# Kernel optimization log

Hardware: AMD Instinct MI355X
Metric: run time of the kernel (lower is better)

Reference implementation:

```python
import jax, jax.numpy as jnp
import numpy as np

B, T, N, A, D, S, E, H = 32, 64, 16, 20, 128, 32, 64, 256  # batch, time, n_agents, n_actions, state_dim, sample_size, embed_dim, hypernet_embed


def _lin(k, fi, fo):
    return jax.random.normal(k, (fi, fo), jnp.float32) / np.sqrt(fi)


def setup_inputs() -> dict:
    key = jax.random.key(0)
    ks = jax.random.split(key, 16)
    batch = B * T
    states = jax.random.normal(ks[0], (B, T, D), jnp.float32)
    a_idx = jax.random.randint(ks[1], (B, T, N), 0, A)
    actions = jax.nn.one_hot(a_idx, A, dtype=jnp.float32)
    agent_qs = jax.random.normal(ks[2], (B, T, N), jnp.float32)
    max_filter = jnp.zeros((B, T, N), jnp.float32)
    # random agent permutations (torch.multinomial without replacement)
    grand_coalitions = jnp.argsort(jax.random.uniform(ks[3], (batch * S, N)), axis=1).astype(jnp.int32)
    return {
        "states": states, "actions": actions, "agent_qs": agent_qs,
        "max_filter": max_filter, "grand_coalitions": grand_coalitions,
        # hyper_w_1: Linear(D,H) -> ReLU -> Linear(H, E*2A)
        "W1a": _lin(ks[4], D, H), "b1a": jnp.zeros((H,), jnp.float32),
        "W1b": _lin(ks[5], H, E * 2 * A), "b1b": jnp.zeros((E * 2 * A,), jnp.float32),
        # hyper_b_1: Linear(D,E)
        "Wb": _lin(ks[6], D, E), "bb": jnp.zeros((E,), jnp.float32),
        # hyper_w_final: Linear(D,H) -> ReLU -> Linear(H,E)
        "Wfa": _lin(ks[7], D, H), "bfa": jnp.zeros((H,), jnp.float32),
        "Wfb": _lin(ks[8], H, E), "bfb": jnp.zeros((E,), jnp.float32),
        # V: Linear(D,E) -> ReLU -> Linear(E,1)
        "Wv1": _lin(ks[9], D, E), "bv1": jnp.zeros((E,), jnp.float32),
        "Wv2": _lin(ks[10], E, 1), "bv2": jnp.zeros((1,), jnp.float32),
    }


def reference(states, actions, agent_qs, max_filter, grand_coalitions,
              W1a, b1a, W1b, b1b, Wb, bb, Wfa, bfa, Wfb, bfb, Wv1, bv1, Wv2, bv2):
    b, t = states.shape[0], states.shape[1]
    batch = b * t
    n, a = actions.shape[2], actions.shape[3]
    s = grand_coalitions.shape[0] // batch
    e = Wb.shape[1]

    st = states.reshape(batch, -1)                      # [batch, D]
    act = actions.reshape(batch, n, a)                  # [batch, N, A]
    gc = grand_coalitions.reshape(batch, s, n)          # [batch, S, N]

    # individual_map one-hot + tril matmul => subcoalition; mask = sub - ind = (j < gc)
    j = jnp.arange(n)
    sub = (j[None, None, None, :] <= gc[..., None]).astype(st.dtype)   # [batch,S,N,N]
    ind = (j[None, None, None, :] == gc[..., None]).astype(st.dtype)
    mask = sub - ind                                                    # [batch,S,i,j]

    # gathered (permuted) actions: perm_act[b,s,j,:] = act[b, gc[b,s,j], :]
    perm_act = act[jnp.arange(batch)[:, None, None], gc]                # [batch,S,N,A]

    # mean over coalition axis j of masked actions, times coalition size, mean over samples
    numer = jnp.einsum('bsij,bsja->bsia', mask, perm_act)               # sum_j masked actions
    cnt = mask.sum(-1)                                                  # [batch,S,N]
    coal = ((numer / n) * cnt[..., None]).mean(axis=1)                  # [batch,N,A]

    # per (batch, agent) hypernetwork mixing
    inputs = jnp.concatenate([coal, act], axis=-1).reshape(batch * n, 2 * a)  # [bn, 2A]
    st_rep = jnp.broadcast_to(st[:, None, :], (batch, n, st.shape[-1])).reshape(batch * n, -1)

    def mlp2(x, Wa_, ba_, Wb_, bb_):
        return jax.nn.relu(x @ Wa_ + ba_) @ Wb_ + bb_

    w1 = jnp.abs(mlp2(st_rep, W1a, b1a, W1b, b1b)).reshape(-1, 2 * a, e)      # [bn,2A,E]
    b1 = (st_rep @ Wb + bb)                                                   # [bn,E]
    hidden = jax.nn.elu(jnp.einsum('bk,bke->be', inputs, w1) + b1)            # [bn,E]
    w_final = jnp.abs(mlp2(st_rep, Wfa, bfa, Wfb, bfb))                       # [bn,E]
    v = jax.nn.relu(st_rep @ Wv1 + bv1) @ Wv2 + bv2                           # [bn,1]
    y = jnp.sum(hidden * w_final, axis=-1, keepdims=True) + v                 # [bn,1]
    w_est = jnp.abs(y).reshape(b, t, n)

    q_tot = jnp.sum(w_est * agent_qs, axis=2, keepdims=True)                  # [B,T,1]
    return q_tot, w_est
```

## Files before the change

kernel.cpp:

```cpp
#include <hip/hip_runtime.h>
#include <math.h>


#define BATCH 2048

typedef __attribute__((ext_vector_type(8))) short bf16x8;
typedef __attribute__((ext_vector_type(4))) float f32x4;

__device__ inline unsigned short f2bf(float f) {
    unsigned int u = __float_as_uint(f);
    unsigned int r = (u + 0x7FFFu + ((u >> 16) & 1u)) >> 16;
    return (unsigned short)r;
}
__device__ inline float bf2f(unsigned short s) {
    return __uint_as_float(((unsigned int)s) << 16);
}

__global__ __launch_bounds__(256) void kPack(
    const float* __restrict__ W1a, const float* __restrict__ b1a,
    const float* __restrict__ Wfa, const float* __restrict__ bfa,
    const float* __restrict__ Wb,  const float* __restrict__ bb,
    const float* __restrict__ Wv1, const float* __restrict__ bv1,
    const float* __restrict__ W1b,
    float* __restrict__ Wcat, float* __restrict__ bcat,
    unsigned short* __restrict__ Bp)
{
    const int t = threadIdx.x, bid = blockIdx.x;
    if (bid < 320) {
        int idx = bid * 256 + t;
        int d = idx / 640, c = idx % 640;
        float v;
        if (c < 256)      v = W1a[d * 256 + c];
        else if (c < 512) v = Wfa[d * 256 + (c - 256)];
        else if (c < 576) v = Wb[d * 64 + (c - 512)];
        else              v = Wv1[d * 64 + (c - 576)];
        Wcat[idx] = v;
        if (idx < 640) {
            int c2 = idx;
            float bv;
            if (c2 < 256)      bv = b1a[c2];
            else if (c2 < 512) bv = bfa[c2 - 256];
            else if (c2 < 576) bv = bb[c2 - 512];
            else               bv = bv1[c2 - 576];
            bcat[c2] = bv;
        }
    } else {
        int idx = (bid - 320) * 256 + t;
        int n_local = idx & 127;
        int g = idx >> 7;
        int kg = g & 3, kcn = g >> 2;
        int kc = kcn & 7, nb = kcn >> 3;
        int kbase = kc * 32 + kg * 8;
        int col = nb * 128 + n_local;
        unsigned short o[8];
        #pragma unroll
        for (int j = 0; j < 8; ++j)
            o[j] = f2bf(W1b[(kbase + j) * 2560 + col]);
        *(uint4*)&Bp[idx * 8] = *(uint4*)o;
    }
}

__global__ __launch_bounds__(256) void kA2(
    const float* __restrict__ X, const float* __restrict__ Wcat,
    const float* __restrict__ bcat,
    unsigned short* __restrict__ h1_bf, float* __restrict__ hf,
    float* __restrict__ b1buf, float* __restrict__ vrelu)
{
    __shared__ float As[16][64];
    __shared__ float Bs[16][64];
    const int tid = threadIdx.x;
    const int tx = tid & 15, ty = tid >> 4;
    const int m0 = blockIdx.y * 64, n0 = blockIdx.x * 64;
    const int lm = tid >> 2, lk = (tid & 3) << 2;
    const int lkk = tid >> 4, lnb = (tid & 15) << 2;

    float c[4][4] = {{0}};
    for (int k0 = 0; k0 < 128; k0 += 16) {
        float4 av = *(const float4*)&X[(m0 + lm) * 128 + k0 + lk];
        As[lk][lm] = av.x; As[lk+1][lm] = av.y; As[lk+2][lm] = av.z; As[lk+3][lm] = av.w;
        *(float4*)&Bs[lkk][lnb] = *(const float4*)&Wcat[(k0 + lkk) * 640 + n0 + lnb];
        __syncthreads();
        #pragma unroll
        for (int kk = 0; kk < 16; ++kk) {
            float4 a4 = *(const float4*)&As[kk][ty * 4];
            float4 b4 = *(const float4*)&Bs[kk][tx * 4];
            float aa[4] = {a4.x, a4.y, a4.z, a4.w};
            float bb4[4] = {b4.x, b4.y, b4.z, b4.w};
            #pragma unroll
            for (int i = 0; i < 4; ++i)
                #pragma unroll
                for (int j = 0; j < 4; ++j)
                    c[i][j] = fmaf(aa[i], bb4[j], c[i][j]);
        }
        __syncthreads();
    }
    const int region = n0 >> 6;
    const int n = n0 + tx * 4;
    float4 bias = *(const float4*)&bcat[n];
    #pragma unroll
    for (int i = 0; i < 4; ++i) {
        int m = m0 + ty * 4 + i;
        float v0 = c[i][0] + bias.x, v1 = c[i][1] + bias.y;
        float v2 = c[i][2] + bias.z, v3 = c[i][3] + bias.w;
        if (region < 4) {
            ushort4 o;
            o.x = f2bf(fmaxf(v0, 0.f)); o.y = f2bf(fmaxf(v1, 0.f));
            o.z = f2bf(fmaxf(v2, 0.f)); o.w = f2bf(fmaxf(v3, 0.f));
            *(ushort4*)&h1_bf[m * 256 + n] = o;
        } else if (region < 8) {
            float4 o = { fmaxf(v0,0.f), fmaxf(v1,0.f), fmaxf(v2,0.f), fmaxf(v3,0.f) };
            *(float4*)&hf[m * 256 + (n - 256)] = o;
        } else if (region == 8) {
            float4 o = { v0, v1, v2, v3 };
            *(float4*)&b1buf[m * 64 + (n - 512)] = o;
        } else {
            float4 o = { fmaxf(v0,0.f), fmaxf(v1,0.f), fmaxf(v2,0.f), fmaxf(v3,0.f) };
            *(float4*)&vrelu[m * 64 + (n - 576)] = o;
        }
    }
}

__global__ __launch_bounds__(320) void kB(
    const float* __restrict__ actions, const int* __restrict__ gc,
    float* __restrict__ coal)
{
    __shared__ int aidx[16];
    __shared__ int q[32][16];
    __shared__ unsigned int msk[32][20];
    const int t = threadIdx.x;
    const int b = blockIdx.x;

    for (int idx = t; idx < 512; idx += 320) ((int*)q)[idx] = gc[b * 512 + idx];
    if (t < 16) {
        int a = 0;
        const float* ap = &actions[(b * 16 + t) * 20];
        for (int k = 0; k < 20; ++k) if (ap[k] > 0.5f) a = k;
        aidx[t] = a;
    }
    for (int idx = t; idx < 640; idx += 320) ((unsigned int*)msk)[idx] = 0u;
    __syncthreads();

    if (t < 32) {
        #pragma unroll
        for (int j = 0; j < 16; ++j) {
            int a = aidx[q[t][j]];
            msk[t][a] |= (1u << j);
        }
    }
    __syncthreads();

    const int i = t / 20, a = t % 20;
    float acc = 0.f;
    #pragma unroll 8
    for (int s = 0; s < 32; ++s) {
        int g = q[s][i];
        acc += (float)(g * __popc(msk[s][a] & ((1u << g) - 1u)));
    }
    coal[b * 320 + t] = acc * (1.0f / 512.0f);
}

__global__ __launch_bounds__(256) void kC2(
    const unsigned short* __restrict__ A, const unsigned short* __restrict__ Bp,
    const float* __restrict__ bias, unsigned short* __restrict__ C)
{
    __shared__ unsigned short As[128 * 32];
    __shared__ unsigned short Bs[4096];
    const int t = threadIdx.x;
    const int lane = t & 63, wave = t >> 6;
    const int ln15 = lane & 15, q4 = lane >> 4;
    const int m0 = blockIdx.y * 128, nb = blockIdx.x, n0 = nb * 128;
    const int wm = (wave & 1) * 64, wn = (wave >> 1) * 64;

    f32x4 acc[4][4];
    #pragma unroll
    for (int i = 0; i < 4; ++i)
        #pragma unroll
        for (int j = 0; j < 4; ++j)
            acc[i][j] = (f32x4){0.f, 0.f, 0.f, 0.f};

    for (int kc = 0; kc < 8; ++kc) {
        #pragma unroll
        for (int c = 0; c < 2; ++c) {
            int ch = t + c * 256;
            int row = ch >> 2, part = ch & 3;
            ((uint4*)As)[ch] = *(const uint4*)&A[(m0 + row) * 256 + kc * 32 + part * 8];
        }
        {
            const uint4* src = (const uint4*)&Bp[(nb * 8 + kc) * 4096];
            ((uint4*)Bs)[t] = src[t];
            ((uint4*)Bs)[t + 256] = src[t + 256];
        }
        __syncthreads();
        bf16x8 af[4], bf[4];
        #pragma unroll
        for (int mi = 0; mi < 4; ++mi)
            af[mi] = *(const bf16x8*)&As[(wm + mi * 16 + ln15) * 32 + q4 * 8];
        #pragma unroll
        for (int ni = 0; ni < 4; ++ni)
            bf[ni] = *(const bf16x8*)&Bs[(q4 * 128 + wn + ni * 16 + ln15) * 8];
        #pragma unroll
        for (int mi = 0; mi < 4; ++mi)
            #pragma unroll
            for (int ni = 0; ni < 4; ++ni)
                acc[mi][ni] = __builtin_amdgcn_mfma_f32_16x16x32_bf16(af[mi], bf[ni], acc[mi][ni], 0, 0, 0);
        __syncthreads();
    }
    #pragma unroll
    for (int ni = 0; ni < 4; ++ni) {
        int col = n0 + wn + ni * 16 + ln15;
        float bv = bias[col];
        #pragma unroll
        for (int mi = 0; mi < 4; ++mi) {
            #pragma unroll
            for (int j = 0; j < 4; ++j) {
                int row = m0 + wm + mi * 16 + q4 * 4 + j;
                C[row * 2560 + col] = f2bf(fabsf(acc[mi][ni][j] + bv));
            }
        }
    }
}

__global__ __launch_bounds__(256) void kSmall(
    const float* __restrict__ hf, const float* __restrict__ Wfb,
    const float* __restrict__ bfb, float* __restrict__ wf)
{
    __shared__ float hfs[8][64];
    __shared__ float wfbs[64][64];
    const int t = threadIdx.x;
    const int e = t & 63, mg = t >> 6;
    const int b0 = blockIdx.x * 8;
    float acc0 = 0.f, acc1 = 0.f;

    for (int kc = 0; kc < 4; ++kc) {
        for (int i = t; i < 1024; i += 256)
            ((float4*)wfbs)[i] = ((const float4*)(Wfb + kc * 64 * 64))[i];
        if (t < 128) {
            int r = t >> 4, p = t & 15;
            ((float4*)hfs)[t] = *(const float4*)&hf[(b0 + r) * 256 + kc * 64 + p * 4];
        }
        __syncthreads();
        #pragma unroll 8
        for (int k = 0; k < 64; ++k) {
            float wv = wfbs[k][e];
            acc0 = fmaf(hfs[mg][k], wv, acc0);
            acc1 = fmaf(hfs[mg + 4][k], wv, acc1);
        }
        __syncthreads();
    }
    float bf = bfb[e];
    wf[(b0 + mg) * 64 + e]     = fabsf(acc0 + bf);
    wf[(b0 + mg + 4) * 64 + e] = fabsf(acc1 + bf);
}

__global__ __launch_bounds__(1024) void kD2(
    const float* __restrict__ coal, const float* __restrict__ actions,
    const unsigned short* __restrict__ w1, const float* __restrict__ b1buf,
    const float* __restrict__ wf, const float* __restrict__ vrelu,
    const float* __restrict__ Wv2, const float* __restrict__ bv2,
    const float* __restrict__ agent_qs, float* __restrict__ out)
{
    __shared__ float ins[16][40];
    __shared__ unsigned short w1s[2560];
    __shared__ float wq[16];
    const int t = threadIdx.x, b = blockIdx.x;

    if (t < 320) {
        ((uint4*)w1s)[t] = ((const uint4*)(w1 + b * 2560))[t];
    } else if (t < 640) {
        int u = t - 320;
        ins[u / 20][u % 20] = coal[b * 320 + u];
    } else if (t < 960) {
        int u = t - 640;
        ins[u / 20][20 + u % 20] = actions[b * 320 + u];
    }
    __syncthreads();

    const int i = t >> 6, e = t & 63;
    float acc = b1buf[b * 64 + e];
    #pragma unroll
    for (int k = 0; k < 40; ++k)
        acc = fmaf(ins[i][k], bf2f(w1s[k * 64 + e]), acc);
    float hidden = acc > 0.f ? acc : expm1f(acc);
    float p = hidden * wf[b * 64 + e] + vrelu[b * 64 + e] * Wv2[e];
    #pragma unroll
    for (int off = 32; off > 0; off >>= 1)
        p += __shfl_down(p, off, 64);
    if (e == 0) {
        float west = fabsf(p + bv2[0]);
        out[2048 + b * 16 + i] = west;
        wq[i] = west * agent_qs[b * 16 + i];
    }
    __syncthreads();
    if (t == 0) {
        float s = 0.f;
        #pragma unroll
        for (int ii = 0; ii < 16; ++ii) s += wq[ii];
        out[b] = s;
    }
}

extern "C" void kernel_launch(void* const* d_in, const int* in_sizes, int n_in,
                              void* d_out, int out_size, void* d_ws, size_t ws_size,
                              hipStream_t stream) {
    const float* states   = (const float*)d_in[0];
    const float* actions  = (const float*)d_in[1];
    const float* agent_qs = (const float*)d_in[2];
    const int*   gc       = (const int*)d_in[4];
    const float* W1a = (const float*)d_in[5];
    const float* b1a = (const float*)d_in[6];
    const float* W1b = (const float*)d_in[7];
    const float* b1b = (const float*)d_in[8];
    const float* Wb  = (const float*)d_in[9];
    const float* bb  = (const float*)d_in[10];
    const float* Wfa = (const float*)d_in[11];
    const float* bfa = (const float*)d_in[12];
    const float* Wfb = (const float*)d_in[13];
    const float* bfb = (const float*)d_in[14];
    const float* Wv1 = (const float*)d_in[15];
    const float* bv1 = (const float*)d_in[16];
    const float* Wv2 = (const float*)d_in[17];
    const float* bv2 = (const float*)d_in[18];

    float* ws     = (float*)d_ws;
    float* Wcat   = ws;
    float* bcat   = Wcat + 81920;
    float* hf     = bcat + 640;
    float* b1buf  = hf + 524288;
    float* vrelu  = b1buf + 131072;
    float* wfbuf  = vrelu + 131072;
    float* coal   = wfbuf + 131072;
    unsigned short* h1_bf = (unsigned short*)(coal + 655360);
    unsigned short* Bp    = h1_bf + 524288;
    unsigned short* w1    = Bp + 655360;
    float* out = (float*)d_out;

    kPack<<<640, 256, 0, stream>>>(W1a, b1a, Wfa, bfa, Wb, bb, Wv1, bv1, W1b,
                                   Wcat, bcat, Bp);
    kB<<<BATCH, 320, 0, stream>>>(actions, gc, coal);
    kA2<<<dim3(10, 32), 256, 0, stream>>>(states, Wcat, bcat, h1_bf, hf, b1buf, vrelu);
    kC2<<<dim3(20, 16), 256, 0, stream>>>(h1_bf, Bp, b1b, w1);
    kSmall<<<256, 256, 0, stream>>>(hf, Wfb, bfb, wfbuf);
    kD2<<<BATCH, 1024, 0, stream>>>(coal, actions, w1, b1buf, wfbuf, vrelu,
                                    Wv2, bv2, agent_qs, out);
}
```

Measured before the change: 156.5 us.

## Merge six kernel launches into three by fusing independent stages

The weight-concatenation pack step is removed, and the state GEMM now reads each weight matrix directly, sharing a launch with the W1b bf16 repacking. The MFMA hypernet GEMM and the small w_final GEMM run as different block ranges of one launch. The coalition-count computation is folded into the final per-batch mixing kernel, so the coal buffer round-trip goes away. The aim is to cut launch overhead and intermediate global traffic. In exchange, the final kernel holds more shared memory and does more serial work per block.

Result: faster. 144.9 us (-7.4%).

```diff
diff --git a/kernel.cpp b/kernel.cpp
--- a/kernel.cpp
+++ b/kernel.cpp
@@ -16,35 +16,22 @@
     return __uint_as_float(((unsigned int)s) << 16);
 }
 
-__global__ __launch_bounds__(256) void kPack(
+__global__ __launch_bounds__(256) void k1(
+    const float* __restrict__ X,
     const float* __restrict__ W1a, const float* __restrict__ b1a,
     const float* __restrict__ Wfa, const float* __restrict__ bfa,
     const float* __restrict__ Wb,  const float* __restrict__ bb,
     const float* __restrict__ Wv1, const float* __restrict__ bv1,
     const float* __restrict__ W1b,
-    float* __restrict__ Wcat, float* __restrict__ bcat,
+    unsigned short* __restrict__ h1_bf, float* __restrict__ hf,
+    float* __restrict__ b1buf, float* __restrict__ vrelu,
     unsigned short* __restrict__ Bp)
 {
+    __shared__ float As[16][64];
+    __shared__ float Bs[16][64];
     const int t = threadIdx.x, bid = blockIdx.x;
-    if (bid < 320) {
-        int idx = bid * 256 + t;
-        int d = idx / 640, c = idx % 640;
-        float v;
-        if (c < 256)      v = W1a[d * 256 + c];
-        else if (c < 512) v = Wfa[d * 256 + (c - 256)];
-        else if (c < 576) v = Wb[d * 64 + (c - 512)];
-        else              v = Wv1[d * 64 + (c - 576)];
-        Wcat[idx] = v;
-        if (idx < 640) {
-            int c2 = idx;
-            float bv;
-            if (c2 < 256)      bv = b1a[c2];
-            else if (c2 < 512) bv = bfa[c2 - 256];
-            else if (c2 < 576) bv = bb[c2 - 512];
-            else               bv = bv1[c2 - 576];
-            bcat[c2] = bv;
-        }
-    } else {
+
+    if (bid >= 320) {
         int idx = (bid - 320) * 256 + t;
         int n_local = idx & 127;
         int g = idx >> 7;
@@ -57,28 +44,26 @@
         for (int j = 0; j < 8; ++j)
             o[j] = f2bf(W1b[(kbase + j) * 2560 + col]);
         *(uint4*)&Bp[idx * 8] = *(uint4*)o;
-    }
-}
-
-__global__ __launch_bounds__(256) void kA2(
-    const float* __restrict__ X, const float* __restrict__ Wcat,
-    const float* __restrict__ bcat,
-    unsigned short* __restrict__ h1_bf, float* __restrict__ hf,
-    float* __restrict__ b1buf, float* __restrict__ vrelu)
-{
-    __shared__ float As[16][64];
-    __shared__ float Bs[16][64];
-    const int tid = threadIdx.x;
-    const int tx = tid & 15, ty = tid >> 4;
-    const int m0 = blockIdx.y * 64, n0 = blockIdx.x * 64;
-    const int lm = tid >> 2, lk = (tid & 3) << 2;
-    const int lkk = tid >> 4, lnb = (tid & 15) << 2;
+        return;
+    }
+
+    const int nb = bid % 10, mb = bid / 10;
+    const int m0 = mb * 64, n0 = nb * 64;
+    const int tx = t & 15, ty = t >> 4;
+    const int lm = t >> 2, lk = (t & 3) << 2;
+    const int lkk = t >> 4, lnb = (t & 15) << 2;
+
+    const float* Wsrc; const float* bsrc; int ldb, c0;
+    if (nb < 4)       { Wsrc = W1a; bsrc = b1a; ldb = 256; c0 = n0; }
+    else if (nb < 8)  { Wsrc = Wfa; bsrc = bfa; ldb = 256; c0 = n0 - 256; }
+    else if (nb == 8) { Wsrc = Wb;  bsrc = bb;  ldb = 64;  c0 = 0; }
+    else              { Wsrc = Wv1; bsrc = bv1; ldb = 64;  c0 = 0; }
 
     float c[4][4] = {{0}};
     for (int k0 = 0; k0 < 128; k0 += 16) {
         float4 av = *(const float4*)&X[(m0 + lm) * 128 + k0 + lk];
         As[lk][lm] = av.x; As[lk+1][lm] = av.y; As[lk+2][lm] = av.z; As[lk+3][lm] = av.w;
-        *(float4*)&Bs[lkk][lnb] = *(const float4*)&Wcat[(k0 + lkk) * 640 + n0 + lnb];
+        *(float4*)&Bs[lkk][lnb] = *(const float4*)&Wsrc[(k0 + lkk) * ldb + c0 + lnb];
         __syncthreads();
         #pragma unroll
         for (int kk = 0; kk < 16; ++kk) {
@@ -94,166 +79,126 @@
         }
         __syncthreads();
     }
-    const int region = n0 >> 6;
-    const int n = n0 + tx * 4;
-    float4 bias = *(const float4*)&bcat[n];
+    const int ncol = c0 + tx * 4;
+    float4 bias = *(const float4*)&bsrc[ncol];
     #pragma unroll
     for (int i = 0; i < 4; ++i) {
         int m = m0 + ty * 4 + i;
         float v0 = c[i][0] + bias.x, v1 = c[i][1] + bias.y;
         float v2 = c[i][2] + bias.z, v3 = c[i][3] + bias.w;
-        if (region < 4) {
+        if (nb < 4) {
             ushort4 o;
             o.x = f2bf(fmaxf(v0, 0.f)); o.y = f2bf(fmaxf(v1, 0.f));
             o.z = f2bf(fmaxf(v2, 0.f)); o.w = f2bf(fmaxf(v3, 0.f));
-            *(ushort4*)&h1_bf[m * 256 + n] = o;
-        } else if (region < 8) {
+            *(ushort4*)&h1_bf[m * 256 + ncol] = o;
+        } else if (nb < 8) {
             float4 o = { fmaxf(v0,0.f), fmaxf(v1,0.f), fmaxf(v2,0.f), fmaxf(v3,0.f) };
-            *(float4*)&hf[m * 256 + (n - 256)] = o;
-        } else if (region == 8) {
+            *(float4*)&hf[m * 256 + ncol] = o;
+        } else if (nb == 8) {
             float4 o = { v0, v1, v2, v3 };
-            *(float4*)&b1buf[m * 64 + (n - 512)] = o;
+            *(float4*)&b1buf[m * 64 + ncol] = o;
         } else {
             float4 o = { fmaxf(v0,0.f), fmaxf(v1,0.f), fmaxf(v2,0.f), fmaxf(v3,0.f) };
-            *(float4*)&vrelu[m * 64 + (n - 576)] = o;
-        }
-    }
-}
-
-__global__ __launch_bounds__(320) void kB(
-    const float* __restrict__ actions, const int* __restrict__ gc,
-    float* __restrict__ coal)
-{
-    __shared__ int aidx[16];
-    __shared__ int q[32][16];
-    __shared__ unsigned int msk[32][20];
-    const int t = threadIdx.x;
-    const int b = blockIdx.x;
-
-    for (int idx = t; idx < 512; idx += 320) ((int*)q)[idx] = gc[b * 512 + idx];
-    if (t < 16) {
-        int a = 0;
-        const float* ap = &actions[(b * 16 + t) * 20];
-        for (int k = 0; k < 20; ++k) if (ap[k] > 0.5f) a = k;
-        aidx[t] = a;
-    }
-    for (int idx = t; idx < 640; idx += 320) ((unsigned int*)msk)[idx] = 0u;
-    __syncthreads();
-
-    if (t < 32) {
-        #pragma unroll
-        for (int j = 0; j < 16; ++j) {
-            int a = aidx[q[t][j]];
-            msk[t][a] |= (1u << j);
-        }
-    }
-    __syncthreads();
-
-    const int i = t / 20, a = t % 20;
-    float acc = 0.f;
-    #pragma unroll 8
-    for (int s = 0; s < 32; ++s) {
-        int g = q[s][i];
-        acc += (float)(g * __popc(msk[s][a] & ((1u << g) - 1u)));
-    }
-    coal[b * 320 + t] = acc * (1.0f / 512.0f);
-}
-
-__global__ __launch_bounds__(256) void kC2(
+            *(float4*)&vrelu[m * 64 + ncol] = o;
+        }
+    }
+}
+
+__global__ __launch_bounds__(256) void k2(
     const unsigned short* __restrict__ A, const unsigned short* __restrict__ Bp,
-    const float* __restrict__ bias, unsigned short* __restrict__ C)
-{
-    __shared__ unsigned short As[128 * 32];
-    __shared__ unsigned short Bs[4096];
-    const int t = threadIdx.x;
-    const int lane = t & 63, wave = t >> 6;
-    const int ln15 = lane & 15, q4 = lane >> 4;
-    const int m0 = blockIdx.y * 128, nb = blockIdx.x, n0 = nb * 128;
-    const int wm = (wave & 1) * 64, wn = (wave >> 1) * 64;
-
-    f32x4 acc[4][4];
-    #pragma unroll
-    for (int i = 0; i < 4; ++i)
-        #pragma unroll
-        for (int j = 0; j < 4; ++j)
-            acc[i][j] = (f32x4){0.f, 0.f, 0.f, 0.f};
-
-    for (int kc = 0; kc < 8; ++kc) {
-        #pragma unroll
-        for (int c = 0; c < 2; ++c) {
-            int ch = t + c * 256;
-            int row = ch >> 2, part = ch & 3;
-            ((uint4*)As)[ch] = *(const uint4*)&A[(m0 + row) * 256 + kc * 32 + part * 8];
-        }
-        {
-            const uint4* src = (const uint4*)&Bp[(nb * 8 + kc) * 4096];
-            ((uint4*)Bs)[t] = src[t];
-            ((uint4*)Bs)[t + 256] = src[t + 256];
-        }
-        __syncthreads();
-        bf16x8 af[4], bf[4];
-        #pragma unroll
-        for (int mi = 0; mi < 4; ++mi)
-            af[mi] = *(const bf16x8*)&As[(wm + mi * 16 + ln15) * 32 + q4 * 8];
-        #pragma unroll
-        for (int ni = 0; ni < 4; ++ni)
-            bf[ni] = *(const bf16x8*)&Bs[(q4 * 128 + wn + ni * 16 + ln15) * 8];
-        #pragma unroll
-        for (int mi = 0; mi < 4; ++mi)
-            #pragma unroll
-            for (int ni = 0; ni < 4; ++ni)
-                acc[mi][ni] = __builtin_amdgcn_mfma_f32_16x16x32_bf16(af[mi], bf[ni], acc[mi][ni], 0, 0, 0);
-        __syncthreads();
-    }
-    #pragma unroll
-    for (int ni = 0; ni < 4; ++ni) {
-        int col = n0 + wn + ni * 16 + ln15;
-        float bv = bias[col];
-        #pragma unroll
-        for (int mi = 0; mi < 4; ++mi) {
-            #pragma unroll
-            for (int j = 0; j < 4; ++j) {
-                int row = m0 + wm + mi * 16 + q4 * 4 + j;
-                C[row * 2560 + col] = f2bf(fabsf(acc[mi][ni][j] + bv));
-            }
-        }
-    }
-}
-
-__global__ __launch_bounds__(256) void kSmall(
+    const float* __restrict__ bias, unsigned short* __restrict__ C,
     const float* __restrict__ hf, const float* __restrict__ Wfb,
     const float* __restrict__ bfb, float* __restrict__ wf)
 {
-    __shared__ float hfs[8][64];
-    __shared__ float wfbs[64][64];
-    const int t = threadIdx.x;
-    const int e = t & 63, mg = t >> 6;
-    const int b0 = blockIdx.x * 8;
-    float acc0 = 0.f, acc1 = 0.f;
-
-    for (int kc = 0; kc < 4; ++kc) {
-        for (int i = t; i < 1024; i += 256)
-            ((float4*)wfbs)[i] = ((const float4*)(Wfb + kc * 64 * 64))[i];
-        if (t < 128) {
-            int r = t >> 4, p = t & 15;
-            ((float4*)hfs)[t] = *(const float4*)&hf[(b0 + r) * 256 + kc * 64 + p * 4];
-        }
-        __syncthreads();
-        #pragma unroll 8
-        for (int k = 0; k < 64; ++k) {
-            float wv = wfbs[k][e];
-            acc0 = fmaf(hfs[mg][k], wv, acc0);
-            acc1 = fmaf(hfs[mg + 4][k], wv, acc1);
-        }
-        __syncthreads();
-    }
-    float bf = bfb[e];
-    wf[(b0 + mg) * 64 + e]     = fabsf(acc0 + bf);
-    wf[(b0 + mg + 4) * 64 + e] = fabsf(acc1 + bf);
-}
-
-__global__ __launch_bounds__(1024) void kD2(
-    const float* __restrict__ coal, const float* __restrict__ actions,
+    __shared__ __align__(16) char smem[18432];
+    const int t = threadIdx.x, bid = blockIdx.x;
+
+    if (bid < 320) {
+        unsigned short* As = (unsigned short*)smem;
+        unsigned short* Bs = (unsigned short*)(smem + 8192);
+        const int lane = t & 63, wave = t >> 6;
+        const int ln15 = lane & 15, q4 = lane >> 4;
+        const int nb = bid % 20, m0 = (bid / 20) * 128, n0 = nb * 128;
+        const int wm = (wave & 1) * 64, wn = (wave >> 1) * 64;
+
+        f32x4 acc[4][4];
+        #pragma unroll
+        for (int i = 0; i < 4; ++i)
+            #pragma unroll
+            for (int j = 0; j < 4; ++j)
+                acc[i][j] = (f32x4){0.f, 0.f, 0.f, 0.f};
+
+        for (int kc = 0; kc < 8; ++kc) {
+            #pragma unroll
+            for (int c = 0; c < 2; ++c) {
+                int ch = t + c * 256;
+                int row = ch >> 2, part = ch & 3;
+                ((uint4*)As)[ch] = *(const uint4*)&A[(m0 + row) * 256 + kc * 32 + part * 8];
+            }
+            {
+                const uint4* src = (const uint4*)&Bp[(nb * 8 + kc) * 4096];
+                ((uint4*)Bs)[t] = src[t];
+                ((uint4*)Bs)[t + 256] = src[t + 256];
+            }
+            __syncthreads();
+            bf16x8 af[4], bfr[4];
+            #pragma unroll
+            for (int mi = 0; mi < 4; ++mi)
+                af[mi] = *(const bf16x8*)&As[(wm + mi * 16 + ln15) * 32 + q4 * 8];
+            #pragma unroll
+            for (int ni = 0; ni < 4; ++ni)
+                bfr[ni] = *(const bf16x8*)&Bs[(q4 * 128 + wn + ni * 16 + ln15) * 8];
+            #pragma unroll
+            for (int mi = 0; mi < 4; ++mi)
+                #pragma unroll
+                for (int ni = 0; ni < 4; ++ni)
+                    acc[mi][ni] = __builtin_amdgcn_mfma_f32_16x16x32_bf16(af[mi], bfr[ni], acc[mi][ni], 0, 0, 0);
+            __syncthreads();
+        }
+        #pragma unroll
+        for (int ni = 0; ni < 4; ++ni) {
+            int col = n0 + wn + ni * 16 + ln15;
+            float bv = bias[col];
+            #pragma unroll
+            for (int mi = 0; mi < 4; ++mi) {
+                #pragma unroll
+                for (int j = 0; j < 4; ++j) {
+                    int row = m0 + wm + mi * 16 + q4 * 4 + j;
+                    C[row * 2560 + col] = f2bf(fabsf(acc[mi][ni][j] + bv));
+                }
+            }
+        }
+    } else {
+        float* hfs  = (float*)smem;
+        float* wfbs = (float*)(smem + 2048);
+        const int e = t & 63, mg = t >> 6;
+        const int b0 = (bid - 320) * 8;
+        float acc0 = 0.f, acc1 = 0.f;
+
+        for (int kc = 0; kc < 4; ++kc) {
+            for (int i = t; i < 1024; i += 256)
+                ((float4*)wfbs)[i] = ((const float4*)(Wfb + kc * 64 * 64))[i];
+            if (t < 128) {
+                int r = t >> 4, p = t & 15;
+                ((float4*)hfs)[t] = *(const float4*)&hf[(b0 + r) * 256 + kc * 64 + p * 4];
+            }
+            __syncthreads();
+            #pragma unroll 8
+            for (int k = 0; k < 64; ++k) {
+                float wv = wfbs[k * 64 + e];
+                acc0 = fmaf(hfs[mg * 64 + k], wv, acc0);
+                acc1 = fmaf(hfs[(mg + 4) * 64 + k], wv, acc1);
+            }
+            __syncthreads();
+        }
+        float bf = bfb[e];
+        wf[(b0 + mg) * 64 + e]     = fabsf(acc0 + bf);
+        wf[(b0 + mg + 4) * 64 + e] = fabsf(acc1 + bf);
+    }
+}
+
+__global__ __launch_bounds__(1024) void k3(
+    const float* __restrict__ actions, const int* __restrict__ gc,
     const unsigned short* __restrict__ w1, const float* __restrict__ b1buf,
     const float* __restrict__ wf, const float* __restrict__ vrelu,
     const float* __restrict__ Wv2, const float* __restrict__ bv2,
@@ -261,6 +206,9 @@
 {
     __shared__ float ins[16][40];
     __shared__ unsigned short w1s[2560];
+    __shared__ int aidx[16];
+    __shared__ int q[32][16];
+    __shared__ unsigned int msk[32][20];
     __shared__ float wq[16];
     const int t = threadIdx.x, b = blockIdx.x;
 
@@ -268,10 +216,32 @@
         ((uint4*)w1s)[t] = ((const uint4*)(w1 + b * 2560))[t];
     } else if (t < 640) {
         int u = t - 320;
-        ins[u / 20][u % 20] = coal[b * 320 + u];
-    } else if (t < 960) {
-        int u = t - 640;
-        ins[u / 20][20 + u % 20] = actions[b * 320 + u];
+        float av = actions[b * 320 + u];
+        ins[u / 20][20 + u % 20] = av;
+        if (av > 0.5f) aidx[u / 20] = u % 20;
+    } else if (t < 768) {
+        ((uint4*)q)[t - 640] = ((const uint4*)(gc + b * 512))[t - 640];
+    } else if (t < 928) {
+        ((uint4*)msk)[t - 768] = make_uint4(0u, 0u, 0u, 0u);
+    }
+    __syncthreads();
+
+    if (t < 32) {
+        #pragma unroll
+        for (int j = 0; j < 16; ++j)
+            msk[t][aidx[q[t][j]]] |= (1u << j);
+    }
+    __syncthreads();
+
+    if (t < 320) {
+        int i = t / 20, a = t % 20;
+        float acc = 0.f;
+        #pragma unroll 8
+        for (int s = 0; s < 32; ++s) {
+            int g = q[s][i];
+            acc += (float)(g * __popc(msk[s][a] & ((1u << g) - 1u)));
+        }
+        ins[i][a] = acc * (1.0f / 512.0f);
     }
     __syncthreads();
 
@@ -322,24 +292,18 @@
     const float* bv2 = (const float*)d_in[18];
 
     float* ws     = (float*)d_ws;
-    float* Wcat   = ws;
-    float* bcat   = Wcat + 81920;
-    float* hf     = bcat + 640;
+    float* hf     = ws;
     float* b1buf  = hf + 524288;
     float* vrelu  = b1buf + 131072;
     float* wfbuf  = vrelu + 131072;
-    float* coal   = wfbuf + 131072;
-    unsigned short* h1_bf = (unsigned short*)(coal + 655360);
+    unsigned short* h1_bf = (unsigned short*)(wfbuf + 131072);
     unsigned short* Bp    = h1_bf + 524288;
     unsigned short* w1    = Bp + 655360;
     float* out = (float*)d_out;
 
-    kPack<<<640, 256, 0, stream>>>(W1a, b1a, Wfa, bfa, Wb, bb, Wv1, bv1, W1b,
-                                   Wcat, bcat, Bp);
-    kB<<<BATCH, 320, 0, stream>>>(actions, gc, coal);
-    kA2<<<dim3(10, 32), 256, 0, stream>>>(states, Wcat, bcat, h1_bf, hf, b1buf, vrelu);
-    kC2<<<dim3(20, 16), 256, 0, stream>>>(h1_bf, Bp, b1b, w1);
-    kSmall<<<256, 256, 0, stream>>>(hf, Wfb, bfb, wfbuf);
-    kD2<<<BATCH, 1024, 0, stream>>>(coal, actions, w1, b1buf, wfbuf, vrelu,
-                                    Wv2, bv2, agent_qs, out);
-}
+    k1<<<640, 256, 0, stream>>>(states, W1a, b1a, Wfa, bfa, Wb, bb, Wv1, bv1,
+                                W1b, h1_bf, hf, b1buf, vrelu, Bp);
+    k2<<<576, 256, 0, stream>>>(h1_bf, Bp, b1b, w1, hf, Wfb, bfb, wfbuf);
+    k3<<<BATCH, 1024, 0, stream>>>(actions, gc, w1, b1buf, wfbuf, vrelu,
+                                   Wv2, bv2, agent_qs, out);
+}
```
